# Performance work log

Hardware: AMD Instinct MI355X
Metric: run time of the kernel (lower is better)

Reference implementation:

```python
import jax, jax.numpy as jnp
import numpy as np
import math

BINS = 32  # quantization_bins


def setup_inputs() -> dict:
    key = jax.random.key(0)
    k1, k2 = jax.random.split(key)
    coords = jax.random.normal(k1, (4, 1024, 2), dtype=jnp.float32)
    # TruncatedNormal(stddev=0.02) init for the learnable table; plain normal*0.02 is fine for a numeric reference
    rpe_table = jax.random.normal(k2, (2 * BINS, 16), dtype=jnp.float32) * 0.02
    return {"coords": coords, "rpe_table": rpe_table}


def reference(coords, rpe_table):
    bins = BINS
    half = bins // 2
    eta = coords[..., 0]  # [B,T]
    phi = coords[..., 1]  # [B,T]
    rel_eta = eta[:, :, None] - eta[:, None, :]  # [B,T,T]
    rel_phi = phi[:, :, None] - phi[:, None, :]  # [B,T,T]
    pi = jnp.asarray(math.pi, dtype=phi.dtype)
    # wrap phi difference to (-pi, pi]; jnp.mod matches tf.math.floormod for floats
    rel_phi = jnp.mod(rel_phi + pi, 2 * pi) - pi
    eta_range = jnp.maximum(jnp.max(jnp.abs(rel_eta)), jnp.asarray(1e-06, eta.dtype))
    phi_range = pi
    # tf.cast float->int32 truncates toward zero, same as astype(int32)
    eta_bins = (rel_eta / eta_range * half).astype(jnp.int32)
    phi_bins = (rel_phi / phi_range * half).astype(jnp.int32)
    eta_bins = jnp.clip(eta_bins, -half, half - 1)
    phi_bins = jnp.clip(phi_bins, -half, half - 1)
    eta_idx = eta_bins + half               # [B,T,T] in [0, bins)
    phi_idx = phi_bins + half + bins        # [B,T,T] in [bins, 2*bins)
    eta_bias = rpe_table[eta_idx]           # [B,T,T,H]
    phi_bias = rpe_table[phi_idx]           # [B,T,T,H]
    bias = eta_bias + phi_bias
    return jnp.transpose(bias, (0, 3, 1, 2))  # [B,H,T,T]
```

## Files before the change

### kernel.cpp

```cpp
#include <hip/hip_runtime.h>
#include <math.h>

#define BB 4
#define TT 1024
#define HH 16
#define NROWS 64
#define RPAD 20
#define ROWS_PER_BLOCK 8

#define PI_F    3.14159265358979323846f
#define TWOPI_F 6.28318530717958647692f

typedef float f4 __attribute__((ext_vector_type(4)));

__global__ __launch_bounds__(256) void QuantizedRPE_fused_kernel(
        const float* __restrict__ coords,
        const float* __restrict__ table,
        float* __restrict__ out) {
    __shared__ float tl[NROWS][RPAD];
    __shared__ float sre[BB];
    int tid = threadIdx.x;
    int lane = tid & 63;
    int w = tid >> 6;

    {
        f4 t4 = ((const f4*)table)[tid];
        int row = tid >> 2, col = (tid & 3) * 4;
        *(f4*)&tl[row][col] = t4;
    }

    {
        const f4* cp4 = (const f4*)coords;
        float mx = -1e30f, mn = 1e30f;
        #pragma unroll
        for (int it = 0; it < TT / 128; ++it) {
            f4 v = cp4[(size_t)w * (TT / 2) + lane + it * 64];
            mx = fmaxf(mx, fmaxf(v.x, v.z));
            mn = fminf(mn, fminf(v.x, v.z));
        }
        #pragma unroll
        for (int m = 32; m; m >>= 1) {
            mx = fmaxf(mx, __shfl_xor(mx, m));
            mn = fminf(mn, __shfl_xor(mn, m));
        }
        if (lane == 0) sre[w] = mx - mn;
    }
    __syncthreads();
    float range = fmaxf(fmaxf(fmaxf(sre[0], sre[1]), fmaxf(sre[2], sre[3])), 1e-6f);

    int b  = blockIdx.x >> 7;
    int i0 = (blockIdx.x & 127) * ROWS_PER_BLOCK;

    float ej[16], pj[16];
    #pragma unroll
    for (int c = 0; c < 4; ++c) {
        const f4* cp = (const f4*)(coords + (size_t)(b * TT + c * 256 + lane * 4) * 2);
        f4 c01 = cp[0];
        f4 c23 = cp[1];
        ej[c * 4 + 0] = c01.x; pj[c * 4 + 0] = c01.y;
        ej[c * 4 + 1] = c01.z; pj[c * 4 + 1] = c01.w;
        ej[c * 4 + 2] = c23.x; pj[c * 4 + 2] = c23.y;
        ej[c * 4 + 3] = c23.z; pj[c * 4 + 3] = c23.w;
    }

    #pragma unroll 1
    for (int r = 0; r < ROWS_PER_BLOCK; ++r) {
        int i = i0 + r;
        float ei  = coords[(size_t)(b * TT + i) * 2 + 0];
        float pii = coords[(size_t)(b * TT + i) * 2 + 1];
        float* rowp = out + ((size_t)(b * HH + 4 * w) * TT + i) * TT + lane * 4;

        #pragma unroll
        for (int c = 0; c < 4; ++c) {
            float v[4][4];
            #pragma unroll
            for (int jj = 0; jj < 4; ++jj) {
                float re = ei - ej[c * 4 + jj];
                int be = (int)(re / range * 16.0f);
                be = min(max(be, -16), 15);
                int eidx = be + 16;
                float ww = (pii - pj[c * 4 + jj]) + PI_F;
                float m = fmodf(ww, TWOPI_F);
                if (m < 0.0f) m += TWOPI_F;
                float rp = m - PI_F;
                int bp = (int)(rp / PI_F * 16.0f);
                bp = min(max(bp, -16), 15);
                int pidx = bp + 48;

                f4 a = *(const f4*)&tl[eidx][4 * w];
                f4 p = *(const f4*)&tl[pidx][4 * w];
                v[jj][0] = a.x + p.x;
                v[jj][1] = a.y + p.y;
                v[jj][2] = a.z + p.z;
                v[jj][3] = a.w + p.w;
            }
            #pragma unroll
            for (int q = 0; q < 4; ++q) {
                f4 sv = { v[0][q], v[1][q], v[2][q], v[3][q] };
                *(f4*)(rowp + (size_t)q * TT * TT + c * 256) = sv;
            }
        }
    }
}

extern "C" void kernel_launch(void* const* d_in, const int* in_sizes, int n_in,
                              void* d_out, int out_size, void* d_ws, size_t ws_size,
                              hipStream_t stream) {
    const float* coords = (const float*)d_in[0];
    const float* table  = (const float*)d_in[1];
    float* out = (float*)d_out;
    (void)d_ws; (void)ws_size;

    QuantizedRPE_fused_kernel<<<BB * TT / ROWS_PER_BLOCK, 256, 0, stream>>>(coords, table, out);
}
```

Baseline: 49.46 us.

## Split heads across blocks and transpose table to per-head layout

Each wave now handles a single head instead of four, with the grid grown fourfold so that block groups cover the four head quarters. The table is stored transposed as [head][row] so each lookup is a scalar LDS read, and each thread writes one float4 per chunk instead of four. This cuts register pressure and per-block work and raises parallelism. The cost is that the index and bin computation, the coordinate loads and the range reduction are each repeated four times across the extra blocks.

Result: slower. 83.55 us (+68.9%).

```diff
diff --git a/kernel.cpp b/kernel.cpp
--- a/kernel.cpp
+++ b/kernel.cpp
@@ -5,7 +5,7 @@
 #define TT 1024
 #define HH 16
 #define NROWS 64
-#define RPAD 20
+#define TPAD 72
 #define ROWS_PER_BLOCK 8
 
 #define PI_F    3.14159265358979323846f
@@ -17,7 +17,7 @@
         const float* __restrict__ coords,
         const float* __restrict__ table,
         float* __restrict__ out) {
-    __shared__ float tl[NROWS][RPAD];
+    __shared__ float tl_t[HH][TPAD];
     __shared__ float sre[BB];
     int tid = threadIdx.x;
     int lane = tid & 63;
@@ -26,7 +26,10 @@
     {
         f4 t4 = ((const f4*)table)[tid];
         int row = tid >> 2, col = (tid & 3) * 4;
-        *(f4*)&tl[row][col] = t4;
+        tl_t[col + 0][row] = t4.x;
+        tl_t[col + 1][row] = t4.y;
+        tl_t[col + 2][row] = t4.z;
+        tl_t[col + 3][row] = t4.w;
     }
 
     {
@@ -48,8 +51,12 @@
     __syncthreads();
     float range = fmaxf(fmaxf(fmaxf(sre[0], sre[1]), fmaxf(sre[2], sre[3])), 1e-6f);
 
-    int b  = blockIdx.x >> 7;
-    int i0 = (blockIdx.x & 127) * ROWS_PER_BLOCK;
+    int b   = blockIdx.x >> 9;
+    int rem = blockIdx.x & 511;
+    int i0  = (rem >> 2) * ROWS_PER_BLOCK;
+    int hq  = rem & 3;
+    int h   = hq * 4 + w;
+    const float* th = &tl_t[h][0];
 
     float ej[16], pj[16];
     #pragma unroll
@@ -68,11 +75,11 @@
         int i = i0 + r;
         float ei  = coords[(size_t)(b * TT + i) * 2 + 0];
         float pii = coords[(size_t)(b * TT + i) * 2 + 1];
-        float* rowp = out + ((size_t)(b * HH + 4 * w) * TT + i) * TT + lane * 4;
+        float* rowp = out + ((size_t)((b * HH + h) * TT + i)) * TT + lane * 4;
 
         #pragma unroll
         for (int c = 0; c < 4; ++c) {
-            float v[4][4];
+            float v[4];
             #pragma unroll
             for (int jj = 0; jj < 4; ++jj) {
                 float re = ei - ej[c * 4 + jj];
@@ -87,18 +94,10 @@
                 bp = min(max(bp, -16), 15);
                 int pidx = bp + 48;
 
-                f4 a = *(const f4*)&tl[eidx][4 * w];
-                f4 p = *(const f4*)&tl[pidx][4 * w];
-                v[jj][0] = a.x + p.x;
-                v[jj][1] = a.y + p.y;
-                v[jj][2] = a.z + p.z;
-                v[jj][3] = a.w + p.w;
+                v[jj] = th[eidx] + th[pidx];
             }
-            #pragma unroll
-            for (int q = 0; q < 4; ++q) {
-                f4 sv = { v[0][q], v[1][q], v[2][q], v[3][q] };
-                *(f4*)(rowp + (size_t)q * TT * TT + c * 256) = sv;
-            }
+            f4 sv = { v[0], v[1], v[2], v[3] };
+            *(f4*)(rowp + c * 256) = sv;
         }
     }
 }
@@ -111,5 +110,5 @@
     float* out = (float*)d_out;
     (void)d_ws; (void)ws_size;
 
-    QuantizedRPE_fused_kernel<<<BB * TT / ROWS_PER_BLOCK, 256, 0, stream>>>(coords, table, out);
+    QuantizedRPE_fused_kernel<<<BB * (TT / ROWS_PER_BLOCK) * 4, 256, 0, stream>>>(coords, table, out);
 }
```
